# Kernel optimization log

Hardware: AMD Instinct MI355X
Metric: run time of the kernel (lower is better)

## Reference

```python
import jax, jax.numpy as jnp
import numpy as np

B, N, DIM = 2, 4096, 1024
HEADS, DH, W = 16, 64, 512
INNER = int(DIM * 2 * 4 / 3)  # 2730 (GEGLU FeedForward, mult=4)


def setup_inputs() -> dict:
    key = jax.random.key(0)
    ks = jax.random.split(key, 6)
    rn = lambda k, shape, sc: jax.random.normal(k, shape, jnp.float32) * sc
    return {
        "x": rn(ks[0], (B, N, DIM), 1.0),
        "ln1_w": jnp.ones((DIM,), jnp.float32),
        "ln1_b": jnp.zeros((DIM,), jnp.float32),
        "w_qkv": rn(ks[1], (DIM, 3 * HEADS * DH), 0.02),
        "w_out": rn(ks[2], (HEADS * DH, DIM), 0.02),
        "ln2_w": jnp.ones((DIM,), jnp.float32),
        "w_ff1": rn(ks[3], (DIM, 2 * INNER), 0.02),
        "w_ff2": rn(ks[4], (INNER, DIM), 0.02),
    }


def _layernorm(x, w, b=None, eps=1e-5):
    m = x.mean(-1, keepdims=True)
    v = x.var(-1, keepdims=True)
    y = (x - m) * jax.lax.rsqrt(v + eps) * w
    return y + b if b is not None else y


def _rotary_freqs(n, d):
    inv = 1.0 / (10000.0 ** (jnp.arange(0, d, 2, dtype=jnp.float32) / d))
    f = jnp.arange(n, dtype=jnp.float32)[:, None] * inv[None, :]  # [n, d/2]
    return jnp.concatenate([f, f], axis=-1)  # [n, d]


def _rotate_half(x):
    x1, x2 = jnp.split(x, 2, axis=-1)
    return jnp.concatenate([-x2, x1], axis=-1)


def _apply_rotary(x, freqs):
    return x * jnp.cos(freqs) + _rotate_half(x) * jnp.sin(freqs)


def reference(x, ln1_w, ln1_b, w_qkv, w_out, ln2_w, w_ff1, w_ff2):
    # ---- LocalMHA (prenorm, causal windowed attention, look_backward=1) ----
    h = _layernorm(x, ln1_w, ln1_b)
    qkv = h @ w_qkv  # [b, n, 3*h*d]
    q, k, v = jnp.split(qkv, 3, axis=-1)
    to_heads = lambda t: t.reshape(B, N, HEADS, DH).transpose(0, 2, 1, 3)  # [b,h,n,d]
    q, k, v = map(to_heads, (q, k, v))

    freqs = _rotary_freqs(N, DH)  # [n, d]
    q = _apply_rotary(q, freqs)
    k = _apply_rotary(k, freqs)
    q = q * (DH ** -0.5)

    nw = N // W
    bq = q.reshape(B, HEADS, nw, W, DH)
    bk = k.reshape(B, HEADS, nw, W, DH)
    bv = v.reshape(B, HEADS, nw, W, DH)

    def look_back(t):  # prepend previous window (zeros for first window)
        prev = jnp.concatenate([jnp.zeros_like(t[:, :, :1]), t[:, :, :-1]], axis=2)
        return jnp.concatenate([prev, t], axis=3)  # [b,h,nw,2w,d]

    kk, vv = look_back(bk), look_back(bv)

    tq = jnp.arange(N).reshape(nw, W)
    tprev = jnp.concatenate([jnp.full((1, W), -1, tq.dtype), tq[:-1]], axis=0)
    tk = jnp.concatenate([tprev, tq], axis=1)  # [nw, 2w]
    mask = (tq[:, :, None] >= tk[:, None, :]) & (tk[:, None, :] >= 0)  # causal + pad

    sim = jnp.einsum('bhnqd,bhnkd->bhnqk', bq, kk)
    sim = jnp.where(mask, sim, jnp.finfo(sim.dtype).min / 2)
    attn = jax.nn.softmax(sim, axis=-1)
    o = jnp.einsum('bhnqk,bhnkd->bhnqd', attn, vv)
    o = o.reshape(B, HEADS, N, DH).transpose(0, 2, 1, 3).reshape(B, N, HEADS * DH)
    x = o @ w_out + x  # residual

    # ---- FeedForward: LN(gamma only) -> GEGLU -> Linear, residual ----
    h = _layernorm(x, ln2_w)
    u = h @ w_ff1
    a, g = jnp.split(u, 2, axis=-1)
    x = (a * jax.nn.gelu(g, approximate=False)) @ w_ff2 + x
    return x
```

## Files before the change

### kernel.cpp

```cpp
#include <hip/hip_runtime.h>
#include <stdint.h>

typedef unsigned short u16;
typedef unsigned int u32;

#define BATCH 2
#define NSEQ  4096
#define DIM   1024
#define HEADS 16
#define DH    64
#define WIN   512
#define INNER 2730
#define ROWS  8192
#define QKV_N 3072
#define FF1_N 5460
#define FF1_NP 5504
#define INNER_P 2752
#define KROT 0.28782313663f

typedef __attribute__((ext_vector_type(8))) short short8;
typedef __attribute__((ext_vector_type(4))) float float4v;

__device__ __forceinline__ float bf2f(u16 u){ union{u32 i;float f;}c; c.i=((u32)u)<<16; return c.f; }
__device__ __forceinline__ u16 f2bf(float f){ union{float f;u32 i;}c; c.f=f; u32 i=c.i;
    return (u16)((i + 0x7FFFu + ((i>>16)&1u))>>16); }

__device__ __forceinline__ float gelu_fast(float g) {
    float t = 0.7978845608f * (g + 0.044715f * g * g * g);
    float th = 1.f - 2.f / (1.f + __expf(2.f * t));
    return 0.5f * g * (1.f + th);
}

__device__ __forceinline__ void gl_lds16(const u16* g, const u16* ldsbase) {
    __builtin_amdgcn_global_load_lds(
        (const __attribute__((address_space(1))) u32*)(uintptr_t)g,
        (__attribute__((address_space(3))) u32*)(uintptr_t)ldsbase,
        16, 0, 0);
}

__device__ __forceinline__ int ff1_src(int n, bool& ok) {
    int t = n >> 7, m = n & 127, j = m >> 4, l = m & 15;
    int p = t * 64 + ((j >> 1) << 4) + l;
    ok = (p < INNER);
    return (j & 1) ? (INNER + p) : p;
}

template <bool REMAP>
__global__ __launch_bounds__(256) void wtrans_kernel(const float* __restrict__ w, u16* __restrict__ wt,
                                                     int K0, int N0, int K1, int N1) {
    __shared__ float tile[32][33];
    int kt = blockIdx.x, nt = blockIdx.y;
    int tx = threadIdx.x & 31, ty = threadIdx.x >> 5;
    int nl = nt * 32 + tx;
    bool ok = (nl < N1);
    int sc = nl;
    if (REMAP) { bool v; sc = ff1_src(nl < N1 ? nl : 0, v); ok = ok && v; }
    else ok = ok && (nl < N0);
#pragma unroll
    for (int yy = 0; yy < 4; yy++) {
        int k = kt*32 + ty + yy*8;
        tile[ty+yy*8][tx] = (k < K0 && ok) ? w[(size_t)k*N0 + sc] : 0.f;
    }
    __syncthreads();
#pragma unroll
    for (int yy = 0; yy < 4; yy++) {
        int n = nt*32 + ty + yy*8, k = kt*32 + tx;
        if (n < N1 && k < K1) wt[(size_t)n*K1 + k] = f2bf(tile[tx][ty+yy*8]);
    }
}

__global__ __launch_bounds__(256) void ln_kernel(const float* __restrict__ x,
                                                 const float* __restrict__ w,
                                                 const float* __restrict__ b,
                                                 u16* __restrict__ out) {
    int row = blockIdx.x;
    const float* xr = x + (size_t)row * DIM;
    int t = threadIdx.x;
    float v[4];
    float s = 0.f, s2 = 0.f;
#pragma unroll
    for (int i = 0; i < 4; i++) {
        float f = xr[t + 256 * i];
        v[i] = f; s += f; s2 += f * f;
    }
#pragma unroll
    for (int off = 32; off; off >>= 1) { s += __shfl_xor(s, off); s2 += __shfl_xor(s2, off); }
    __shared__ float ls[10];
    int wave = t >> 6, lane = t & 63;
    if (lane == 0) { ls[wave] = s; ls[4 + wave] = s2; }
    __syncthreads();
    if (t == 0) {
        float ts  = ls[0] + ls[1] + ls[2] + ls[3];
        float ts2 = ls[4] + ls[5] + ls[6] + ls[7];
        float mean = ts * (1.f / DIM);
        float var  = ts2 * (1.f / DIM) - mean * mean;
        ls[8] = mean; ls[9] = 1.f / sqrtf(var + 1e-5f);
    }
    __syncthreads();
    float mean = ls[8], inv = ls[9];
    u16* orow = out + (size_t)row * DIM;
#pragma unroll
    for (int i = 0; i < 4; i++) {
        int c = t + 256 * i;
        float y = (v[i] - mean) * inv * w[c];
        if (b) y += b[c];
        orow[c] = f2bf(y);
    }
}

template <int MODE>
__global__ __launch_bounds__(256) void gemm_tile(const u16* __restrict__ A,
                                                 const u16* __restrict__ Bt,
                                                 const float* __restrict__ resid,
                                                 void* __restrict__ Cv,
                                                 int M, int N, int K) {
    __shared__ u16 As[128 * 32];
    __shared__ u16 Bs[128 * 32];
    int tiles_n = N >> 7;
    int gs  = tiles_n << 3;
    int gid = blockIdx.x / gs;
    int loc = blockIdx.x % gs;
    int tm = gid * 8 + (loc & 7);
    int tn = loc >> 3;
    int tid = threadIdx.x, wave = tid >> 6, lane = tid & 63;
    int quad = lane >> 4, l15 = lane & 15;
    int wm = wave >> 1, wn = wave & 1;
    int srow = wave * 32 + (lane >> 2);
    int sgrp = (lane & 3) ^ ((srow >> 1) & 3);
    const u16* Ag = A  + (size_t)(tm * 128 + srow) * K + sgrp * 8;
    const u16* Bg = Bt + (size_t)(tn * 128 + srow) * K + sgrp * 8;
    const u16* Alb = &As[wave * 1024];
    const u16* Blb = &Bs[wave * 1024];
    int rg = (l15 >> 1) & 3;
    float4v acc[4][4];
#pragma unroll
    for (int i = 0; i < 4; i++)
#pragma unroll
        for (int j = 0; j < 4; j++) acc[i][j] = (float4v){0.f, 0.f, 0.f, 0.f};
    for (int k0 = 0; k0 < K; k0 += 32) {
        __syncthreads();
        gl_lds16(Ag + k0,                 Alb);
        gl_lds16(Ag + (size_t)16*K + k0,  Alb + 512);
        gl_lds16(Bg + k0,                 Blb);
        gl_lds16(Bg + (size_t)16*K + k0,  Blb + 512);
        __syncthreads();
        short8 af[4], bf[4];
#pragma unroll
        for (int i = 0; i < 4; i++)
            af[i] = *(const short8*)&As[(wm*64 + i*16 + l15)*32 + ((quad ^ rg) * 8)];
#pragma unroll
        for (int j = 0; j < 4; j++)
            bf[j] = *(const short8*)&Bs[(wn*64 + j*16 + l15)*32 + ((quad ^ rg) * 8)];
#pragma unroll
        for (int i = 0; i < 4; i++)
#pragma unroll
            for (int j = 0; j < 4; j++)
                acc[i][j] = __builtin_amdgcn_mfma_f32_16x16x32_bf16(af[i], bf[j], acc[i][j], 0, 0, 0);
    }
    if (MODE == 3) {
        u16* ag = (u16*)Cv;
#pragma unroll
        for (int i = 0; i < 4; i++) {
#pragma unroll
            for (int r = 0; r < 4; r++) {
                size_t row = (size_t)(tm*128 + wm*64 + i*16 + quad*4 + r);
#pragma unroll
                for (int jp = 0; jp < 2; jp++) {
                    float a = acc[i][2*jp][r];
                    float g = acc[i][2*jp+1][r];
                    int col = tn*64 + wn*32 + jp*16 + l15;
                    ag[row * INNER_P + col] = f2bf(a * gelu_fast(g));
                }
            }
        }
        return;
    }
    if (MODE == 2) {
        u16* C = (u16*)Cv;
        int sector = tn >> 3;
        if (sector < 2) {
            float inv0 = __expf(-(float)l15 * KROT);
            float inv1 = __expf(-(float)(l15 + 16) * KROT);
            float sc = (sector == 0) ? 0.125f : 1.0f;
#pragma unroll
            for (int i = 0; i < 4; i++) {
#pragma unroll
                for (int r = 0; r < 4; r++) {
                    int row = tm*128 + wm*64 + i*16 + quad*4 + r;
                    float fn = (float)(row & (NSEQ - 1));
                    float s0, c0, s1, c1;
                    __sincosf(fn * inv0, &s0, &c0);
                    __sincosf(fn * inv1, &s1, &c1);
                    float a0 = acc[i][0][r], a1 = acc[i][1][r];
                    float a2 = acc[i][2][r], a3 = acc[i][3][r];
                    size_t base = (size_t)row * N + tn*128 + wn*64 + l15;
                    C[base]      = f2bf((a0*c0 - a2*s0) * sc);
                    C[base + 16] = f2bf((a1*c1 - a3*s1) * sc);
                    C[base + 32] = f2bf((a2*c0 + a0*s0) * sc);
                    C[base + 48] = f2bf((a3*c1 + a1*s1) * sc);
                }
            }
        } else {
#pragma unroll
            for (int i = 0; i < 4; i++)
#pragma unroll
                for (int r = 0; r < 4; r++) {
                    size_t base = (size_t)(tm*128 + wm*64 + i*16 + quad*4 + r) * N + tn*128 + wn*64 + l15;
#pragma unroll
                    for (int j = 0; j < 4; j++) C[base + j*16] = f2bf(acc[i][j][r]);
                }
        }
        return;
    }
#pragma unroll
    for (int i = 0; i < 4; i++) {
#pragma unroll
        for (int r = 0; r < 4; r++) {
            size_t row = (size_t)(tm*128 + wm*64 + i*16 + quad*4 + r);
#pragma unroll
            for (int j = 0; j < 4; j++) {
                int col = tn*128 + wn*64 + j*16 + l15;
                size_t idx = row * N + col;
                float v = acc[i][j][r];
                if (MODE == 1) { if (resid) v += resid[idx]; ((float*)Cv)[idx] = v; }
                else ((u16*)Cv)[idx] = f2bf(v);
            }
        }
    }
}

__global__ __launch_bounds__(256) void vtrans_kernel(const u16* __restrict__ qkv, u16* __restrict__ vt) {
    __shared__ u16 tile[64][72];
    int t = threadIdx.x;
    int n0 = (blockIdx.x & 63) * 64;
    int hh = (blockIdx.x >> 6) & 15;
    int b  = blockIdx.x >> 10;
    int r = t >> 2, cb = (t & 3) * 16;
    const u16* src = qkv + (size_t)(b * NSEQ + n0 + r) * QKV_N + 2 * DIM + hh * 64 + cb;
    uint4 v0 = *(const uint4*)(src);
    uint4 v1 = *(const uint4*)(src + 8);
    *(uint4*)&tile[r][cb]     = v0;
    *(uint4*)&tile[r][cb + 8] = v1;
    __syncthreads();
    int d = t >> 2, nb = (t & 3) * 16;
    __align__(16) u16 vals[16];
#pragma unroll
    for (int e = 0; e < 16; e++) vals[e] = tile[nb + e][d];
    u16* dst = vt + ((size_t)(b * HEADS + hh) * DH + d) * NSEQ + n0 + nb;
    *(uint4*)(dst)     = *(uint4*)&vals[0];
    *(uint4*)(dst + 8) = *(uint4*)&vals[8];
}

__global__ __launch_bounds__(256) void attn_kernel(const u16* __restrict__ qkv,
                                                   const u16* __restrict__ vt,
                                                   u16* __restrict__ o) {
    __shared__ u16 Ks[128 * 64];
    __shared__ u16 Vs[64 * 128];
    __shared__ u16 p_lds[4][16][136];
    int tid = threadIdx.x, wave = tid >> 6, lane = tid & 63;
    int quad = lane >> 4, l15 = lane & 15;
    int bi = blockIdx.x;
    int qb = bi & 7, w0 = (bi >> 3) & 7, hh = (bi >> 6) & 15, b = bi >> 10;
    int qt = qb * 4 + wave;
    int qlocal = qt * 16 + l15;
    const u16* qp = qkv + (size_t)(b*NSEQ + w0*WIN + qt*16 + l15) * QKV_N + hh*64 + quad*8;
    short8 bq0 = *(const short8*)(qp);
    short8 bq1 = *(const short8*)(qp + 32);
    int krow0 = b * NSEQ + (w0 - 1) * WIN;
    const u16* vbase = vt + (size_t)(b * HEADS + hh) * DH * NSEQ + (w0 - 1) * WIN;
    int ks_row = lane >> 3;
    int ks_g   = (lane & 7) ^ ks_row;
    int vs_row = lane >> 4;
    int vs_j0  = lane & 15;
    int swz = l15 & 7;
    float m_ = -1e30f, l_ = 0.f;
    float4v O[4] = {{0,0,0,0},{0,0,0,0},{0,0,0,0},{0,0,0,0}};
    int cstart = (w0 == 0) ? 4 : 0;
    int clast  = (512 + qb * 64 + 63) >> 7;
    u16 (*pt)[136] = p_lds[wave];
    for (int c = cstart; c <= clast; c++) {
        int kb = c * 128;
        __syncthreads();
#pragma unroll
        for (int i = 0; i < 4; i++) {
            int kloc = wave * 32 + i * 8 + ks_row;
            gl_lds16(qkv + (size_t)(krow0 + kb + kloc) * QKV_N + DIM + hh*64 + ks_g*8,
                     &Ks[(wave*32 + i*8) * 64]);
        }
#pragma unroll
        for (int i = 0; i < 4; i++) {
            int dloc = wave * 16 + i * 4 + vs_row;
            int jsrc = vs_j0 ^ (dloc & 7);
            gl_lds16(vbase + (size_t)dloc * NSEQ + kb + jsrc * 8,
                     &Vs[(wave*16 + i*4) * 128]);
        }
        __syncthreads();
        float4v s[8];
#pragma unroll
        for (int t = 0; t < 8; t++) {
            int krow = (t*16 + l15) * 64;
            short8 ka0 = *(const short8*)&Ks[krow + ((quad    ) ^ swz) * 8];
            short8 ka1 = *(const short8*)&Ks[krow + ((quad + 4) ^ swz) * 8];
            float4v st = {0.f, 0.f, 0.f, 0.f};
            st = __builtin_amdgcn_mfma_f32_16x16x32_bf16(ka0, bq0, st, 0, 0, 0);
            st = __builtin_amdgcn_mfma_f32_16x16x32_bf16(ka1, bq1, st, 0, 0, 0);
            int ck = kb + t*16 + quad*4;
#pragma unroll
            for (int r = 0; r < 4; r++)
                if (ck + r >= 512 && ck + r - 512 > qlocal) st[r] = -1e30f;
            s[t] = st;
        }
        float mc = -1e30f;
#pragma unroll
        for (int t = 0; t < 8; t++)
#pragma unroll
            for (int r = 0; r < 4; r++) mc = fmaxf(mc, s[t][r]);
        mc = fmaxf(mc, __shfl_xor(mc, 16));
        mc = fmaxf(mc, __shfl_xor(mc, 32));
        float mn = fmaxf(m_, mc);
        float alpha = __expf(m_ - mn);
        m_ = mn;
        float su = 0.f;
#pragma unroll
        for (int t = 0; t < 8; t++) {
            union { u16 h[4]; uint2 v; } pk;
#pragma unroll
            for (int r = 0; r < 4; r++) {
                float p = __expf(s[t][r] - mn);
                su += p;
                pk.h[r] = f2bf(p);
            }
            *(uint2*)&pt[l15][t*16 + quad*4] = pk.v;
        }
        su += __shfl_xor(su, 16);
        su += __shfl_xor(su, 32);
        l_ = l_ * alpha + su;
#pragma unroll
        for (int t = 0; t < 4; t++)
#pragma unroll
            for (int r = 0; r < 4; r++) O[t][r] *= alpha;
#pragma unroll
        for (int g = 0; g < 4; g++) {
            short8 pf = *(const short8*)&pt[l15][g*32 + quad*8];
#pragma unroll
            for (int t = 0; t < 4; t++) {
                short8 vf = *(const short8*)&Vs[(t*16 + l15) * 128 + ((g*4 + quad) ^ swz) * 8];
                O[t] = __builtin_amdgcn_mfma_f32_16x16x32_bf16(vf, pf, O[t], 0, 0, 0);
            }
        }
    }
    float inv = 1.f / l_;
    u16* op = o + (size_t)(b*NSEQ + w0*WIN + qt*16 + l15) * DIM + hh*64;
#pragma unroll
    for (int t = 0; t < 4; t++) {
        union { u16 h[4]; uint2 v; } pk;
#pragma unroll
        for (int r = 0; r < 4; r++) pk.h[r] = f2bf(O[t][r] * inv);
        *(uint2*)(op + t*16 + quad*4) = pk.v;
    }
}

extern "C" void kernel_launch(void* const* d_in, const int* in_sizes, int n_in,
                              void* d_out, int out_size, void* d_ws, size_t ws_size,
                              hipStream_t stream) {
    const float* x      = (const float*)d_in[0];
    const float* ln1_w  = (const float*)d_in[1];
    const float* ln1_b  = (const float*)d_in[2];
    const float* w_qkv  = (const float*)d_in[3];
    const float* w_out  = (const float*)d_in[4];
    const float* ln2_w  = (const float*)d_in[5];
    const float* w_ff1  = (const float*)d_in[6];
    const float* w_ff2  = (const float*)d_in[7];
    float* out = (float*)d_out;

    char* ws = (char*)d_ws;
    size_t off = 0;
    auto alloc = [&](size_t bytes) { size_t o = off; off += (bytes + 255) & ~(size_t)255; return o; };
    size_t off_wqt  = alloc((size_t)QKV_N  * DIM * 2);
    size_t off_wot  = alloc((size_t)DIM    * DIM * 2);
    size_t off_wf1t = alloc((size_t)FF1_NP * DIM * 2);
    size_t off_wf2t = alloc((size_t)DIM    * INNER_P * 2);
    size_t off_h    = alloc((size_t)ROWS * DIM * 2);
    size_t sz_qkv = (size_t)ROWS * QKV_N * 2;
    size_t sz_vt  = (size_t)BATCH * HEADS * DH * NSEQ * 2;
    size_t off_qkv  = alloc(sz_qkv);
    size_t off_vt   = alloc(sz_vt);
    size_t off_o    = alloc((size_t)ROWS * DIM * 2);
    size_t off_x1   = alloc((size_t)ROWS * DIM * 4);
    size_t off_ag   = alloc((size_t)ROWS * INNER_P * 2);

    u16* wqt  = (u16*)(ws + off_wqt);
    u16* wot  = (u16*)(ws + off_wot);
    u16* wf1t = (u16*)(ws + off_wf1t);
    u16* wf2t = (u16*)(ws + off_wf2t);
    u16* h    = (u16*)(ws + off_h);
    u16* qkv  = (u16*)(ws + off_qkv);
    u16* vt   = (u16*)(ws + off_vt);
    u16* o    = (u16*)(ws + off_o);
    float* x1 = (float*)(ws + off_x1);
    u16* ag   = (u16*)(ws + off_ag);

    wtrans_kernel<false><<<dim3(32, 96),  256, 0, stream>>>(w_qkv, wqt,  DIM,   QKV_N, DIM,     QKV_N);
    wtrans_kernel<false><<<dim3(32, 32),  256, 0, stream>>>(w_out, wot,  DIM,   DIM,   DIM,     DIM);
    wtrans_kernel<true ><<<dim3(32, 172), 256, 0, stream>>>(w_ff1, wf1t, DIM,   FF1_N, DIM,     FF1_NP);
    wtrans_kernel<false><<<dim3(86, 32),  256, 0, stream>>>(w_ff2, wf2t, INNER, DIM,   INNER_P, DIM);

    ln_kernel<<<ROWS, 256, 0, stream>>>(x, ln1_w, ln1_b, h);
    gemm_tile<2><<<(ROWS/128) * (QKV_N/128), 256, 0, stream>>>(h, wqt, nullptr, qkv, ROWS, QKV_N, DIM);
    vtrans_kernel<<<BATCH * HEADS * (NSEQ / 64), 256, 0, stream>>>(qkv, vt);
    attn_kernel<<<BATCH * HEADS * 8 * 8, 256, 0, stream>>>(qkv, vt, o);
    gemm_tile<1><<<(ROWS/128) * (DIM/128), 256, 0, stream>>>(o, wot, x, x1, ROWS, DIM, DIM);
    ln_kernel<<<ROWS, 256, 0, stream>>>(x1, ln2_w, nullptr, h);
    gemm_tile<3><<<(ROWS/128) * (FF1_NP/128), 256, 0, stream>>>(h, wf1t, nullptr, ag, ROWS, FF1_NP, DIM);
    gemm_tile<1><<<(ROWS/128) * (DIM/128), 256, 0, stream>>>(ag, wf2t, x1, out, ROWS, DIM, INNER_P);

    (void)in_sizes; (void)n_in; (void)out_size; (void)ws_size;
}
```

Before: 579.0 us.

## Double-buffer LDS tiles in GEMM to overlap global loads with MFMA

```diff
diff --git a/kernel.cpp b/kernel.cpp
--- a/kernel.cpp
+++ b/kernel.cpp
@@ -114,8 +114,8 @@
                                                  const float* __restrict__ resid,
                                                  void* __restrict__ Cv,
                                                  int M, int N, int K) {
-    __shared__ u16 As[128 * 32];
-    __shared__ u16 Bs[128 * 32];
+    __shared__ u16 As[2][128 * 32];
+    __shared__ u16 Bs[2][128 * 32];
     int tiles_n = N >> 7;
     int gs  = tiles_n << 3;
     int gid = blockIdx.x / gs;
@@ -129,33 +129,50 @@
     int sgrp = (lane & 3) ^ ((srow >> 1) & 3);
     const u16* Ag = A  + (size_t)(tm * 128 + srow) * K + sgrp * 8;
     const u16* Bg = Bt + (size_t)(tn * 128 + srow) * K + sgrp * 8;
-    const u16* Alb = &As[wave * 1024];
-    const u16* Blb = &Bs[wave * 1024];
+    const u16* Alb0 = &As[0][wave * 1024];
+    const u16* Blb0 = &Bs[0][wave * 1024];
+    const u16* Alb1 = &As[1][wave * 1024];
+    const u16* Blb1 = &Bs[1][wave * 1024];
     int rg = (l15 >> 1) & 3;
     float4v acc[4][4];
 #pragma unroll
     for (int i = 0; i < 4; i++)
 #pragma unroll
         for (int j = 0; j < 4; j++) acc[i][j] = (float4v){0.f, 0.f, 0.f, 0.f};
-    for (int k0 = 0; k0 < K; k0 += 32) {
-        __syncthreads();
-        gl_lds16(Ag + k0,                 Alb);
-        gl_lds16(Ag + (size_t)16*K + k0,  Alb + 512);
-        gl_lds16(Bg + k0,                 Blb);
-        gl_lds16(Bg + (size_t)16*K + k0,  Blb + 512);
-        __syncthreads();
+
+    gl_lds16(Ag,                Alb0);
+    gl_lds16(Ag + (size_t)16*K, Alb0 + 512);
+    gl_lds16(Bg,                Blb0);
+    gl_lds16(Bg + (size_t)16*K, Blb0 + 512);
+    __syncthreads();
+
+    int nk = K >> 5;
+    for (int t = 0; t < nk; ++t) {
+        int buf = t & 1;
+        if (t + 1 < nk) {
+            int k0 = (t + 1) << 5;
+            const u16* Al = buf ? Alb0 : Alb1;
+            const u16* Bl = buf ? Blb0 : Blb1;
+            gl_lds16(Ag + k0,                Al);
+            gl_lds16(Ag + (size_t)16*K + k0, Al + 512);
+            gl_lds16(Bg + k0,                Bl);
+            gl_lds16(Bg + (size_t)16*K + k0, Bl + 512);
+        }
+        const u16* Asb = &As[buf][0];
+        const u16* Bsb = &Bs[buf][0];
         short8 af[4], bf[4];
 #pragma unroll
         for (int i = 0; i < 4; i++)
-            af[i] = *(const short8*)&As[(wm*64 + i*16 + l15)*32 + ((quad ^ rg) * 8)];
+            af[i] = *(const short8*)&Asb[(wm*64 + i*16 + l15)*32 + ((quad ^ rg) * 8)];
 #pragma unroll
         for (int j = 0; j < 4; j++)
-            bf[j] = *(const short8*)&Bs[(wn*64 + j*16 + l15)*32 + ((quad ^ rg) * 8)];
+            bf[j] = *(const short8*)&Bsb[(wn*64 + j*16 + l15)*32 + ((quad ^ rg) * 8)];
 #pragma unroll
         for (int i = 0; i < 4; i++)
 #pragma unroll
             for (int j = 0; j < 4; j++)
                 acc[i][j] = __builtin_amdgcn_mfma_f32_16x16x32_bf16(af[i], bf[j], acc[i][j], 0, 0, 0);
+        __syncthreads();
     }
     if (MODE == 3) {
         u16* ag = (u16*)Cv;
```

Result: faster. 544.1 us (-6.0%).
